# Kernel tuning notes

Hardware: AMD Instinct MI355X
Metric: run time of the kernel (lower is better)

The kernel has to match this reference:

```python
import jax, jax.numpy as jnp
import numpy as np

N = 100000   # nodes
E = 1600000  # edges
NF, EF = 128, 16      # node_features, edge_features
NFIL, EFIL = 64, 32   # node_filters, edge_filters
C = 16                # classes


def setup_inputs() -> dict:
    key = jax.random.key(0)
    ks = jax.random.split(key, 12)
    s = 0.1
    return {
        "x": jax.random.normal(ks[0], (N, NF), jnp.float32),
        "edge_index": jax.random.randint(ks[1], (2, E), 0, N),
        "edge_x": jax.random.normal(ks[2], (E, EF), jnp.float32),
        # edge MLP params
        "W1": jax.random.normal(ks[3], (EF, EFIL), jnp.float32) * s,
        "b1": jnp.zeros((EFIL,), jnp.float32),
        "W2": jax.random.normal(ks[4], (EFIL, 1), jnp.float32) * s,
        "b2": jnp.zeros((1,), jnp.float32),
        # GCN layer params
        "Wc1": jax.random.normal(ks[5], (NF, NFIL), jnp.float32) * s,
        "bc1": jnp.zeros((NFIL,), jnp.float32),
        "Wc2": jax.random.normal(ks[6], (NFIL, C), jnp.float32) * s,
        "bc2": jnp.zeros((C,), jnp.float32),
    }


def gcn_conv(x, src, tgt, w, W, b, n):
    # PyG GCNConv with edge_weight: x @ W, symmetric norm, scatter-add, + bias.
    x = x @ W                                             # [n, out]
    deg = jax.ops.segment_sum(w, tgt, num_segments=n)     # weighted degree incl. self-loops
    dinv = jnp.where(deg > 0, jax.lax.rsqrt(deg), 0.0)
    norm = dinv[src] * w * dinv[tgt]                      # [E+n]
    out = jax.ops.segment_sum(norm[:, None] * x[src], tgt, num_segments=n)
    return out + b


def reference(x, edge_index, edge_x, W1, b1, W2, b2, Wc1, bc1, Wc2, bc2):
    # edge MLP -> scalar attention weight per edge
    h = jax.nn.relu(edge_x @ W1 + b1)
    ew = jax.nn.sigmoid(h @ W2 + b2).reshape(-1)          # [E]
    src, tgt = edge_index[0], edge_index[1]
    # add self-loops with weight 1 (as GCNConv does internally)
    loop = jnp.arange(N)
    src_f = jnp.concatenate([src, loop])
    tgt_f = jnp.concatenate([tgt, loop])
    ew_f = jnp.concatenate([ew, jnp.ones((N,), ew.dtype)])
    h1 = jax.nn.relu(gcn_conv(x, src_f, tgt_f, ew_f, Wc1, bc1, N))
    # dropout omitted: eval mode (F.dropout is identity when training=False)
    h2 = gcn_conv(h1, src_f, tgt_f, ew_f, Wc2, bc2, N)
    return jax.nn.log_softmax(h2, axis=1)
```

## Files before the change

### kernel.cpp

```cpp
#include <hip/hip_runtime.h>
#include <math.h>

#define NFD 128
#define EF_ 16
#define EFIL 32
#define NFIL 64
#define CLS 16

typedef unsigned int uint;
typedef unsigned long long ull;
typedef unsigned short ushort;

__device__ inline void fma4(float4& a, float s, const float4& w) {
  a.x = fmaf(s, w.x, a.x); a.y = fmaf(s, w.y, a.y);
  a.z = fmaf(s, w.z, a.z); a.w = fmaf(s, w.w, a.w);
}

__device__ inline uint bf16_rn(float f) {
  uint u = __float_as_uint(f);
  return (u + 0x7FFFu + ((u >> 16) & 1u)) >> 16;
}
__device__ inline float entw(uint lo) {
  return __uint_as_float((lo >> 17) << 16);
}

__global__ __launch_bounds__(256) void edge_mlp_link_kernel(
    const float* __restrict__ edge_x, const int* __restrict__ ei,
    const float* __restrict__ W1, const float* __restrict__ b1,
    const float* __restrict__ W2, const float* __restrict__ b2,
    int* __restrict__ head, ull* __restrict__ nextbuf, int E) {
  __shared__ __align__(16) float sW1[EF_ * EFIL];
  __shared__ float sb1[EFIL];
  __shared__ float sW2[EFIL];
  __shared__ float sb2v;
  int t = threadIdx.x;
  for (int idx = t; idx < EF_ * EFIL / 4; idx += 256)
    reinterpret_cast<float4*>(sW1)[idx] = reinterpret_cast<const float4*>(W1)[idx];
  if (t < EFIL) { sb1[t] = b1[t]; sW2[t] = W2[t]; }
  if (t == 64) sb2v = b2[0];
  __syncthreads();
  int e = blockIdx.x * 256 + t;
  if (e >= E) return;
  int sv = ei[e], tg = ei[(size_t)E + e];
  int old = atomicExch(&head[(size_t)tg * 8 + (blockIdx.x & 7)], e);
  const float4* ex4 = reinterpret_cast<const float4*>(edge_x) + (size_t)e * (EF_ / 4);
  float ex[EF_];
  #pragma unroll
  for (int q = 0; q < EF_ / 4; q++) {
    float4 v = ex4[q];
    ex[4*q+0] = v.x; ex[4*q+1] = v.y; ex[4*q+2] = v.z; ex[4*q+3] = v.w;
  }
  float acc[EFIL];
  #pragma unroll
  for (int j = 0; j < EFIL; j++) acc[j] = sb1[j];
  #pragma unroll
  for (int k = 0; k < EF_; k++) {
    float xk = ex[k];
    #pragma unroll
    for (int j4 = 0; j4 < EFIL / 4; j4++) {
      float4 w = reinterpret_cast<const float4*>(sW1)[k * (EFIL/4) + j4];
      acc[4*j4+0] = fmaf(xk, w.x, acc[4*j4+0]);
      acc[4*j4+1] = fmaf(xk, w.y, acc[4*j4+1]);
      acc[4*j4+2] = fmaf(xk, w.z, acc[4*j4+2]);
      acc[4*j4+3] = fmaf(xk, w.w, acc[4*j4+3]);
    }
  }
  float s = sb2v;
  #pragma unroll
  for (int j = 0; j < EFIL; j++) s = fmaf(fmaxf(acc[j], 0.f), sW2[j], s);
  float sig = 1.0f / (1.0f + __expf(-s));
  uint lo = ((bf16_rn(sig) & 0x7FFFu) << 17) | (uint)sv;
  nextbuf[e] = ((ull)(uint)old << 32) | lo;
}

__global__ __launch_bounds__(256) void walk_kernel(
    const int* __restrict__ head, const ull* __restrict__ nextbuf,
    uint* __restrict__ slotc, int* __restrict__ grp_cnt,
    float* __restrict__ dinv, int caprows, int n) {
  int i = blockIdx.x * blockDim.x + threadIdx.x;
  if (i >= n) return;
  int4 ha = *reinterpret_cast<const int4*>(head + (size_t)i * 8);
  int4 hb = *reinterpret_cast<const int4*>(head + (size_t)i * 8 + 4);
  int ev0 = ha.x, ev1 = ha.y, ev2 = ha.z, ev3 = ha.w;
  int ev4 = hb.x, ev5 = hb.y, ev6 = hb.z, ev7 = hb.w;
  int cnt = 0;
  float sum = 0.f;
  bool any = ev0 >= 0 || ev1 >= 0 || ev2 >= 0 || ev3 >= 0 ||
             ev4 >= 0 || ev5 >= 0 || ev6 >= 0 || ev7 >= 0;
  while (any) {
    ull v0 = 0, v1 = 0, v2 = 0, v3 = 0, v4 = 0, v5 = 0, v6 = 0, v7 = 0;
    if (ev0 >= 0) v0 = nextbuf[ev0];
    if (ev1 >= 0) v1 = nextbuf[ev1];
    if (ev2 >= 0) v2 = nextbuf[ev2];
    if (ev3 >= 0) v3 = nextbuf[ev3];
    if (ev4 >= 0) v4 = nextbuf[ev4];
    if (ev5 >= 0) v5 = nextbuf[ev5];
    if (ev6 >= 0) v6 = nextbuf[ev6];
    if (ev7 >= 0) v7 = nextbuf[ev7];
    #define STEP(EV, VV)                                              \
    if (EV >= 0) {                                                    \
      uint lo = (uint)VV; sum += entw(lo);                            \
      if (cnt < caprows) slotc[(size_t)cnt * n + i] = lo;             \
      cnt++; EV = (int)(uint)(VV >> 32);                              \
    }
    STEP(ev0, v0) STEP(ev1, v1) STEP(ev2, v2) STEP(ev3, v3)
    STEP(ev4, v4) STEP(ev5, v5) STEP(ev6, v6) STEP(ev7, v7)
    #undef STEP
    any = ev0 >= 0 || ev1 >= 0 || ev2 >= 0 || ev3 >= 0 ||
          ev4 >= 0 || ev5 >= 0 || ev6 >= 0 || ev7 >= 0;
  }
  grp_cnt[i] = min(cnt, caprows);
  dinv[i] = rsqrtf(1.0f + sum);
}

__global__ __launch_bounds__(256) void gemm1_kernel(
    const float* __restrict__ x, const float* __restrict__ Wc1,
    uint* __restrict__ xwb, int n) {
  __shared__ __align__(16) float sW[NFD * NFIL];
  int t = threadIdx.x;
  for (int idx = t; idx < NFD * NFIL / 4; idx += 256)
    reinterpret_cast<float4*>(sW)[idx] = reinterpret_cast<const float4*>(Wc1)[idx];
  __syncthreads();
  int tc = t & 15;
  int tr = t >> 4;
  int nrb = (n + 31) >> 5;
  const float4* sW4 = reinterpret_cast<const float4*>(sW);
  for (int rb = blockIdx.x; rb < nrb; rb += gridDim.x) {
    int r0 = rb * 32 + tr * 2;
    int r1 = r0 + 1;
    int c0 = r0 < n ? r0 : n - 1;
    int c1 = r1 < n ? r1 : n - 1;
    const float4* xr0 = reinterpret_cast<const float4*>(x + (size_t)c0 * NFD);
    const float4* xr1 = reinterpret_cast<const float4*>(x + (size_t)c1 * NFD);
    float4 a0 = {0, 0, 0, 0}, a1 = {0, 0, 0, 0};
    #pragma unroll 4
    for (int k4 = 0; k4 < NFD / 4; k4++) {
      float4 xa = xr0[k4];
      float4 xb = xr1[k4];
      float4 w0 = sW4[(k4*4+0)*16 + tc];
      float4 w1 = sW4[(k4*4+1)*16 + tc];
      float4 w2 = sW4[(k4*4+2)*16 + tc];
      float4 w3 = sW4[(k4*4+3)*16 + tc];
      fma4(a0, xa.x, w0); fma4(a0, xa.y, w1); fma4(a0, xa.z, w2); fma4(a0, xa.w, w3);
      fma4(a1, xb.x, w0); fma4(a1, xb.y, w1); fma4(a1, xb.z, w2); fma4(a1, xb.w, w3);
    }
    if (r0 < n) {
      uint2 o = {bf16_rn(a0.x) | (bf16_rn(a0.y) << 16),
                 bf16_rn(a0.z) | (bf16_rn(a0.w) << 16)};
      reinterpret_cast<uint2*>(xwb + (size_t)r0 * 32)[tc] = o;
    }
    if (r1 < n) {
      uint2 o = {bf16_rn(a1.x) | (bf16_rn(a1.y) << 16),
                 bf16_rn(a1.z) | (bf16_rn(a1.w) << 16)};
      reinterpret_cast<uint2*>(xwb + (size_t)r1 * 32)[tc] = o;
    }
  }
}

__global__ __launch_bounds__(256) void agg1_fused_kernel(
    const int* __restrict__ grp_cnt, const uint* __restrict__ slotc,
    const float* __restrict__ dinv, const uint* __restrict__ xwb,
    const float* __restrict__ bc1, const float* __restrict__ Wc2,
    ushort* __restrict__ ywb, int n) {
  __shared__ float sh[16][NFIL + 4];
  __shared__ float sW2[NFIL * CLS];
  __shared__ float sb1[NFIL];
  int t = threadIdx.x;
  for (int i = t; i < NFIL * CLS; i += 256) sW2[i] = Wc2[i];
  if (t < NFIL) sb1[t] = bc1[t];
  __syncthreads();
  int r = t >> 4;
  int node = blockIdx.x * 16 + r;
  int f4 = t & 15;
  bool ok = node < n;
  int nd = ok ? node : 0;
  int cnt = ok ? grp_cnt[nd] : 0;
  const uint2* xw2 = reinterpret_cast<const uint2*>(xwb);
  float d = ok ? dinv[nd] : 0.f;
  uint2 g = xw2[(size_t)nd * 16 + f4];
  float4 acc = {d * __uint_as_float(g.x << 16),
                d * __uint_as_float(g.x & 0xFFFF0000u),
                d * __uint_as_float(g.y << 16),
                d * __uint_as_float(g.y & 0xFFFF0000u)};
  #define A1STEP(VV)                                                  \
  {                                                                   \
    int s_ = VV & 0x1FFFF;                                            \
    float w_ = entw(VV) * dinv[s_];                                   \
    uint2 g_ = xw2[(size_t)s_ * 16 + f4];                             \
    acc.x = fmaf(w_, __uint_as_float(g_.x << 16), acc.x);             \
    acc.y = fmaf(w_, __uint_as_float(g_.x & 0xFFFF0000u), acc.y);     \
    acc.z = fmaf(w_, __uint_as_float(g_.y << 16), acc.z);             \
    acc.w = fmaf(w_, __uint_as_float(g_.y & 0xFFFF0000u), acc.w);     \
  }
  int p = 0;
  for (; p + 3 < cnt; p += 4) {
    uint v0 = slotc[(size_t)p * n + nd];
    uint v1 = slotc[(size_t)(p + 1) * n + nd];
    uint v2 = slotc[(size_t)(p + 2) * n + nd];
    uint v3 = slotc[(size_t)(p + 3) * n + nd];
    A1STEP(v0) A1STEP(v1) A1STEP(v2) A1STEP(v3)
  }
  for (; p < cnt; p++) {
    uint v0 = slotc[(size_t)p * n + nd];
    A1STEP(v0)
  }
  #undef A1STEP
  sh[r][4*f4 + 0] = fmaxf(fmaf(d, acc.x, sb1[4*f4 + 0]), 0.f);
  sh[r][4*f4 + 1] = fmaxf(fmaf(d, acc.y, sb1[4*f4 + 1]), 0.f);
  sh[r][4*f4 + 2] = fmaxf(fmaf(d, acc.z, sb1[4*f4 + 2]), 0.f);
  sh[r][4*f4 + 3] = fmaxf(fmaf(d, acc.w, sb1[4*f4 + 3]), 0.f);
  __syncthreads();
  {
    int j = t & 15;
    float o = 0.f;
    #pragma unroll
    for (int k = 0; k < NFIL; k++) o = fmaf(sh[r][k], sW2[k * CLS + j], o);
    if (ok) ywb[(size_t)node * CLS + j] = (ushort)bf16_rn(d * o);
  }
}

__global__ __launch_bounds__(256) void agg2_fused_kernel(
    const int* __restrict__ grp_cnt, const uint* __restrict__ slotc,
    const float* __restrict__ dinv, const ushort* __restrict__ ywb,
    const float* __restrict__ bc2, float* __restrict__ out, int n) {
  __shared__ float sb2[CLS];
  int t = threadIdx.x;
  if (t < CLS) sb2[t] = bc2[t];
  __syncthreads();
  int node = blockIdx.x * 16 + (t >> 4);
  int j = t & 15;
  bool ok = node < n;
  int nd = ok ? node : 0;
  int cnt = ok ? grp_cnt[nd] : 0;
  float d = ok ? dinv[nd] : 0.f;
  float acc = __uint_as_float((uint)ywb[(size_t)nd * CLS + j] << 16);
  #define A2STEP(VV)                                                       \
  {                                                                        \
    int s_ = VV & 0x1FFFF;                                                 \
    acc = fmaf(entw(VV),                                                   \
               __uint_as_float((uint)ywb[(size_t)s_ * CLS + j] << 16),     \
               acc);                                                       \
  }
  int p = 0;
  for (; p + 3 < cnt; p += 4) {
    uint v0 = slotc[(size_t)p * n + nd];
    uint v1 = slotc[(size_t)(p + 1) * n + nd];
    uint v2 = slotc[(size_t)(p + 2) * n + nd];
    uint v3 = slotc[(size_t)(p + 3) * n + nd];
    A2STEP(v0) A2STEP(v1) A2STEP(v2) A2STEP(v3)
  }
  for (; p < cnt; p++) {
    uint v0 = slotc[(size_t)p * n + nd];
    A2STEP(v0)
  }
  #undef A2STEP
  float v = fmaf(d, acc, sb2[j]);
  float m = v;
  m = fmaxf(m, __shfl_xor(m, 1, 16));
  m = fmaxf(m, __shfl_xor(m, 2, 16));
  m = fmaxf(m, __shfl_xor(m, 4, 16));
  m = fmaxf(m, __shfl_xor(m, 8, 16));
  float ex = __expf(v - m);
  float ssum = ex;
  ssum += __shfl_xor(ssum, 1, 16);
  ssum += __shfl_xor(ssum, 2, 16);
  ssum += __shfl_xor(ssum, 4, 16);
  ssum += __shfl_xor(ssum, 8, 16);
  if (ok) out[(size_t)node * CLS + j] = (v - m) - __logf(ssum);
}

extern "C" void kernel_launch(void* const* d_in, const int* in_sizes, int n_in,
                              void* d_out, int out_size, void* d_ws, size_t ws_size,
                              hipStream_t stream) {
  const float* x      = (const float*)d_in[0];
  const int*   ei     = (const int*)d_in[1];
  const float* edge_x = (const float*)d_in[2];
  const float* W1     = (const float*)d_in[3];
  const float* b1     = (const float*)d_in[4];
  const float* W2     = (const float*)d_in[5];
  const float* b2     = (const float*)d_in[6];
  const float* Wc1    = (const float*)d_in[7];
  const float* bc1    = (const float*)d_in[8];
  const float* Wc2    = (const float*)d_in[9];
  const float* bc2    = (const float*)d_in[10];
  float* outp = (float*)d_out;
  int n = in_sizes[0] / NFD;
  int E = in_sizes[1] / 2;

  int cap = 48;
  while (cap > 32 && 8.0 * E + (double)n * (200.0 + 4.0 * cap) > (double)ws_size)
    cap -= 8;

  char* base = (char*)d_ws;
  int* head = (int*)base;            base += (size_t)n * 32;
  ull* nextbuf = (ull*)base;         base += (size_t)E * 8;
  uint* slotc = (uint*)base;         base += (size_t)n * cap * 4;
  int* grp_cnt = (int*)base;         base += (size_t)n * 4;
  float* dinv = (float*)base;        base += (size_t)n * 4;
  uint* xwb = (uint*)base;           base += (size_t)n * 128;
  ushort* ywb = (ushort*)base;

  int NBE = (E + 255) / 256;
  int nblk16 = (n + 15) / 16;
  int nblk256 = (n + 255) / 256;
  hipMemsetAsync(head, 0xFF, (size_t)n * 32, stream);
  edge_mlp_link_kernel<<<NBE, 256, 0, stream>>>(
      edge_x, ei, W1, b1, W2, b2, head, nextbuf, E);
  walk_kernel<<<nblk256, 256, 0, stream>>>(head, nextbuf, slotc, grp_cnt, dinv, cap, n);
  gemm1_kernel<<<1024, 256, 0, stream>>>(x, Wc1, xwb, n);
  agg1_fused_kernel<<<nblk16, 256, 0, stream>>>(grp_cnt, slotc, dinv, xwb, bc1, Wc2, ywb, n);
  agg2_fused_kernel<<<nblk16, 256, 0, stream>>>(grp_cnt, slotc, dinv, ywb, bc2, outp, n);
}
```

Measured before the change: 214.4 us.

## Fuse linked-list walk and first GEMM into one kernel with interleaved phases

Merges the latency-bound per-node edge-list walk and the x@Wc1 GEMM into a single 1024-block launch. Odd blocks run the GEMM first and even blocks run the walk first, so pointer chasing can overlap with streaming FMA work on the same CUs. GEMM work is redistributed to per-wave 8-row tiles. Walk coverage now relies on 1024*256 threads being at least n, which holds for this problem size but is a silent limit. Every block also loads the 32 KB Wc1 tile into shared memory, including blocks whose walk share is empty.

```diff
diff --git a/kernel.cpp b/kernel.cpp
--- a/kernel.cpp
+++ b/kernel.cpp
@@ -73,86 +73,93 @@
   nextbuf[e] = ((ull)(uint)old << 32) | lo;
 }
 
-__global__ __launch_bounds__(256) void walk_kernel(
+__global__ __launch_bounds__(256) void walk_gemm_kernel(
     const int* __restrict__ head, const ull* __restrict__ nextbuf,
     uint* __restrict__ slotc, int* __restrict__ grp_cnt,
-    float* __restrict__ dinv, int caprows, int n) {
-  int i = blockIdx.x * blockDim.x + threadIdx.x;
-  if (i >= n) return;
-  int4 ha = *reinterpret_cast<const int4*>(head + (size_t)i * 8);
-  int4 hb = *reinterpret_cast<const int4*>(head + (size_t)i * 8 + 4);
-  int ev0 = ha.x, ev1 = ha.y, ev2 = ha.z, ev3 = ha.w;
-  int ev4 = hb.x, ev5 = hb.y, ev6 = hb.z, ev7 = hb.w;
-  int cnt = 0;
-  float sum = 0.f;
-  bool any = ev0 >= 0 || ev1 >= 0 || ev2 >= 0 || ev3 >= 0 ||
-             ev4 >= 0 || ev5 >= 0 || ev6 >= 0 || ev7 >= 0;
-  while (any) {
-    ull v0 = 0, v1 = 0, v2 = 0, v3 = 0, v4 = 0, v5 = 0, v6 = 0, v7 = 0;
-    if (ev0 >= 0) v0 = nextbuf[ev0];
-    if (ev1 >= 0) v1 = nextbuf[ev1];
-    if (ev2 >= 0) v2 = nextbuf[ev2];
-    if (ev3 >= 0) v3 = nextbuf[ev3];
-    if (ev4 >= 0) v4 = nextbuf[ev4];
-    if (ev5 >= 0) v5 = nextbuf[ev5];
-    if (ev6 >= 0) v6 = nextbuf[ev6];
-    if (ev7 >= 0) v7 = nextbuf[ev7];
-    #define STEP(EV, VV)                                              \
-    if (EV >= 0) {                                                    \
-      uint lo = (uint)VV; sum += entw(lo);                            \
-      if (cnt < caprows) slotc[(size_t)cnt * n + i] = lo;             \
-      cnt++; EV = (int)(uint)(VV >> 32);                              \
-    }
-    STEP(ev0, v0) STEP(ev1, v1) STEP(ev2, v2) STEP(ev3, v3)
-    STEP(ev4, v4) STEP(ev5, v5) STEP(ev6, v6) STEP(ev7, v7)
-    #undef STEP
-    any = ev0 >= 0 || ev1 >= 0 || ev2 >= 0 || ev3 >= 0 ||
-          ev4 >= 0 || ev5 >= 0 || ev6 >= 0 || ev7 >= 0;
-  }
-  grp_cnt[i] = min(cnt, caprows);
-  dinv[i] = rsqrtf(1.0f + sum);
-}
-
-__global__ __launch_bounds__(256) void gemm1_kernel(
+    float* __restrict__ dinv, int caprows, int n,
     const float* __restrict__ x, const float* __restrict__ Wc1,
-    uint* __restrict__ xwb, int n) {
+    uint* __restrict__ xwb) {
   __shared__ __align__(16) float sW[NFD * NFIL];
   int t = threadIdx.x;
+  int bid = blockIdx.x;
   for (int idx = t; idx < NFD * NFIL / 4; idx += 256)
     reinterpret_cast<float4*>(sW)[idx] = reinterpret_cast<const float4*>(Wc1)[idx];
   __syncthreads();
-  int tc = t & 15;
-  int tr = t >> 4;
-  int nrb = (n + 31) >> 5;
-  const float4* sW4 = reinterpret_cast<const float4*>(sW);
-  for (int rb = blockIdx.x; rb < nrb; rb += gridDim.x) {
-    int r0 = rb * 32 + tr * 2;
-    int r1 = r0 + 1;
-    int c0 = r0 < n ? r0 : n - 1;
-    int c1 = r1 < n ? r1 : n - 1;
-    const float4* xr0 = reinterpret_cast<const float4*>(x + (size_t)c0 * NFD);
-    const float4* xr1 = reinterpret_cast<const float4*>(x + (size_t)c1 * NFD);
-    float4 a0 = {0, 0, 0, 0}, a1 = {0, 0, 0, 0};
-    #pragma unroll 4
-    for (int k4 = 0; k4 < NFD / 4; k4++) {
-      float4 xa = xr0[k4];
-      float4 xb = xr1[k4];
-      float4 w0 = sW4[(k4*4+0)*16 + tc];
-      float4 w1 = sW4[(k4*4+1)*16 + tc];
-      float4 w2 = sW4[(k4*4+2)*16 + tc];
-      float4 w3 = sW4[(k4*4+3)*16 + tc];
-      fma4(a0, xa.x, w0); fma4(a0, xa.y, w1); fma4(a0, xa.z, w2); fma4(a0, xa.w, w3);
-      fma4(a1, xb.x, w0); fma4(a1, xb.y, w1); fma4(a1, xb.z, w2); fma4(a1, xb.w, w3);
-    }
-    if (r0 < n) {
-      uint2 o = {bf16_rn(a0.x) | (bf16_rn(a0.y) << 16),
-                 bf16_rn(a0.z) | (bf16_rn(a0.w) << 16)};
-      reinterpret_cast<uint2*>(xwb + (size_t)r0 * 32)[tc] = o;
-    }
-    if (r1 < n) {
-      uint2 o = {bf16_rn(a1.x) | (bf16_rn(a1.y) << 16),
-                 bf16_rn(a1.z) | (bf16_rn(a1.w) << 16)};
-      reinterpret_cast<uint2*>(xwb + (size_t)r1 * 32)[tc] = o;
+  bool gemm_first = (bid & 1) != 0;
+
+  for (int phase = 0; phase < 2; phase++) {
+    if ((phase == 0) == gemm_first) {
+      int gw = bid * 4 + (t >> 6);
+      int nwaves = gridDim.x * 4;
+      int l = t & 63, tc = l & 15, tr = l >> 4;
+      int ntile = (n + 7) >> 3;
+      const float4* sW4 = reinterpret_cast<const float4*>(sW);
+      for (int tile = gw; tile < ntile; tile += nwaves) {
+        int r0 = tile * 8 + tr * 2;
+        int r1 = r0 + 1;
+        int c0 = r0 < n ? r0 : n - 1;
+        int c1 = r1 < n ? r1 : n - 1;
+        const float4* xr0 = reinterpret_cast<const float4*>(x + (size_t)c0 * NFD);
+        const float4* xr1 = reinterpret_cast<const float4*>(x + (size_t)c1 * NFD);
+        float4 a0 = {0, 0, 0, 0}, a1 = {0, 0, 0, 0};
+        #pragma unroll 4
+        for (int k4 = 0; k4 < NFD / 4; k4++) {
+          float4 xa = xr0[k4];
+          float4 xb = xr1[k4];
+          float4 w0 = sW4[(k4*4+0)*16 + tc];
+          float4 w1 = sW4[(k4*4+1)*16 + tc];
+          float4 w2 = sW4[(k4*4+2)*16 + tc];
+          float4 w3 = sW4[(k4*4+3)*16 + tc];
+          fma4(a0, xa.x, w0); fma4(a0, xa.y, w1); fma4(a0, xa.z, w2); fma4(a0, xa.w, w3);
+          fma4(a1, xb.x, w0); fma4(a1, xb.y, w1); fma4(a1, xb.z, w2); fma4(a1, xb.w, w3);
+        }
+        if (r0 < n) {
+          uint2 o = {bf16_rn(a0.x) | (bf16_rn(a0.y) << 16),
+                     bf16_rn(a0.z) | (bf16_rn(a0.w) << 16)};
+          reinterpret_cast<uint2*>(xwb + (size_t)r0 * 32)[tc] = o;
+        }
+        if (r1 < n) {
+          uint2 o = {bf16_rn(a1.x) | (bf16_rn(a1.y) << 16),
+                     bf16_rn(a1.z) | (bf16_rn(a1.w) << 16)};
+          reinterpret_cast<uint2*>(xwb + (size_t)r1 * 32)[tc] = o;
+        }
+      }
+    } else {
+      int i = bid * 256 + t;
+      if (i < n) {
+        int4 ha = *reinterpret_cast<const int4*>(head + (size_t)i * 8);
+        int4 hb = *reinterpret_cast<const int4*>(head + (size_t)i * 8 + 4);
+        int ev0 = ha.x, ev1 = ha.y, ev2 = ha.z, ev3 = ha.w;
+        int ev4 = hb.x, ev5 = hb.y, ev6 = hb.z, ev7 = hb.w;
+        int cnt = 0;
+        float sum = 0.f;
+        bool any = ev0 >= 0 || ev1 >= 0 || ev2 >= 0 || ev3 >= 0 ||
+                   ev4 >= 0 || ev5 >= 0 || ev6 >= 0 || ev7 >= 0;
+        while (any) {
+          ull v0 = 0, v1 = 0, v2 = 0, v3 = 0, v4 = 0, v5 = 0, v6 = 0, v7 = 0;
+          if (ev0 >= 0) v0 = nextbuf[ev0];
+          if (ev1 >= 0) v1 = nextbuf[ev1];
+          if (ev2 >= 0) v2 = nextbuf[ev2];
+          if (ev3 >= 0) v3 = nextbuf[ev3];
+          if (ev4 >= 0) v4 = nextbuf[ev4];
+          if (ev5 >= 0) v5 = nextbuf[ev5];
+          if (ev6 >= 0) v6 = nextbuf[ev6];
+          if (ev7 >= 0) v7 = nextbuf[ev7];
+          #define STEP(EV, VV)                                              \
+          if (EV >= 0) {                                                    \
+            uint lo = (uint)VV; sum += entw(lo);                            \
+            if (cnt < caprows) slotc[(size_t)cnt * n + i] = lo;             \
+            cnt++; EV = (int)(uint)(VV >> 32);                              \
+          }
+          STEP(ev0, v0) STEP(ev1, v1) STEP(ev2, v2) STEP(ev3, v3)
+          STEP(ev4, v4) STEP(ev5, v5) STEP(ev6, v6) STEP(ev7, v7)
+          #undef STEP
+          any = ev0 >= 0 || ev1 >= 0 || ev2 >= 0 || ev3 >= 0 ||
+                ev4 >= 0 || ev5 >= 0 || ev6 >= 0 || ev7 >= 0;
+        }
+        grp_cnt[i] = min(cnt, caprows);
+        dinv[i] = rsqrtf(1.0f + sum);
+      }
     }
   }
 }
@@ -302,12 +309,11 @@
 
   int NBE = (E + 255) / 256;
   int nblk16 = (n + 15) / 16;
-  int nblk256 = (n + 255) / 256;
   hipMemsetAsync(head, 0xFF, (size_t)n * 32, stream);
   edge_mlp_link_kernel<<<NBE, 256, 0, stream>>>(
       edge_x, ei, W1, b1, W2, b2, head, nextbuf, E);
-  walk_kernel<<<nblk256, 256, 0, stream>>>(head, nextbuf, slotc, grp_cnt, dinv, cap, n);
-  gemm1_kernel<<<1024, 256, 0, stream>>>(x, Wc1, xwb, n);
+  walk_gemm_kernel<<<1024, 256, 0, stream>>>(
+      head, nextbuf, slotc, grp_cnt, dinv, cap, n, x, Wc1, xwb);
   agg1_fused_kernel<<<nblk16, 256, 0, stream>>>(grp_cnt, slotc, dinv, xwb, bc1, Wc2, ywb, n);
   agg2_fused_kernel<<<nblk16, 256, 0, stream>>>(grp_cnt, slotc, dinv, ywb, bc2, outp, n);
 }
```

After: 202.6 us. 5.5% less time.
